# Kernel optimization log

Measured on AMD Instinct MI355X. Metric: run time of the kernel, lower is better.

Reference implementation:

```python
import jax, jax.numpy as jnp
import numpy as np

N_NODES = 100000
N_GRAPHS = 64
EPS = 1e-5


def _sage_conv(x, src, dst, Wl, bl, Wr):
    # mean-aggregate neighbor messages (src -> dst), then lin_l(agg) + lin_r(x)
    n = x.shape[0]
    deg = jax.ops.segment_sum(jnp.ones_like(dst, dtype=x.dtype), dst, num_segments=n)
    agg = jax.ops.segment_sum(x[src], dst, num_segments=n)  # [N, d]
    agg = agg / jnp.maximum(deg, 1.0)[:, None]
    return agg @ Wl + bl + x @ Wr


def _bn_relu(x, gamma, beta):
    mu = jnp.mean(x, axis=0)
    var = jnp.var(x, axis=0)
    return jax.nn.relu((x - mu) * jax.lax.rsqrt(var + EPS) * gamma + beta)


def setup_inputs() -> dict:
    key = jax.random.key(0)
    ks = jax.random.split(key, 16)
    E = 1600000
    x = jax.random.normal(ks[0], (N_NODES, 2), dtype=jnp.float32)
    edge_index = jax.random.randint(ks[1], (2, E), 0, N_NODES, dtype=jnp.int64)
    batch = jnp.sort(jax.random.randint(ks[2], (N_NODES,), 0, N_GRAPHS, dtype=jnp.int64))

    def lin(k, din, dout):
        s = 1.0 / np.sqrt(din)
        return jax.random.uniform(k, (din, dout), jnp.float32, -s, s)

    d = {"x": x, "edge_index": edge_index, "batch": batch}
    dims = [(2, 32), (32, 64), (64, 128)]
    for i, (din, dout) in enumerate(dims, 1):
        k1, k2 = jax.random.split(ks[2 + i])
        d[f"Wl{i}"] = lin(k1, din, dout)
        d[f"bl{i}"] = jnp.zeros((dout,), jnp.float32)
        d[f"Wr{i}"] = lin(k2, din, dout)
        d[f"g{i}"] = jnp.ones((dout,), jnp.float32)
        d[f"be{i}"] = jnp.zeros((dout,), jnp.float32)
    d["Wf1"] = lin(ks[10], 128, 64)
    d["bf1"] = jnp.zeros((64,), jnp.float32)
    d["Wf2"] = lin(ks[11], 64, 1)
    d["bf2"] = jnp.zeros((1,), jnp.float32)
    return d


def reference(x, edge_index, batch,
              Wl1, bl1, Wr1, g1, be1,
              Wl2, bl2, Wr2, g2, be2,
              Wl3, bl3, Wr3, g3, be3,
              Wf1, bf1, Wf2, bf2):
    src, dst = edge_index[0], edge_index[1]
    h = _bn_relu(_sage_conv(x, src, dst, Wl1, bl1, Wr1), g1, be1)
    h = _bn_relu(_sage_conv(h, src, dst, Wl2, bl2, Wr2), g2, be2)
    h = _bn_relu(_sage_conv(h, src, dst, Wl3, bl3, Wr3), g3, be3)
    # global mean pool over graphs
    cnt = jax.ops.segment_sum(jnp.ones_like(batch, dtype=h.dtype), batch, num_segments=N_GRAPHS)
    pooled = jax.ops.segment_sum(h, batch, num_segments=N_GRAPHS) / jnp.maximum(cnt, 1.0)[:, None]
    out = jax.nn.relu(pooled @ Wf1 + bf1)
    # dropout is identity in eval mode
    return out @ Wf2 + bf2
```

## Files before the change

### kernel.cpp

```cpp
#include <hip/hip_runtime.h>
#include <hip/hip_fp16.h>

#define N_NODES 100000
#define N_GRAPHS 64
#define BN_EPS 1e-5

#define NB 782
#define NC 49
#define PT1 4096
#define PT2 2048
#define BPC 16
#define CAP 3072

__device__ __forceinline__ float bfly64(float v) {
#pragma unroll
    for (int m = 1; m < 64; m <<= 1) v += __shfl_xor(v, m, 64);
    return v;
}

__device__ __forceinline__ unsigned pack_h2(float a, float b) {
    __half2 h = __floats2half2_rn(a, b);
    unsigned w;
    __builtin_memcpy(&w, &h, 4);
    return w;
}

__device__ __forceinline__ float2 unpack_h2(unsigned w) {
    __half2 h;
    __builtin_memcpy(&h, &w, 4);
    return __half22float2(h);
}

__global__ void hist_fine(const int* __restrict__ dst, int* __restrict__ bhist, int E) {
    __shared__ int h[NB];
    for (int i = threadIdx.x; i < NB; i += 256) h[i] = 0;
    __syncthreads();
    int stride = gridDim.x * 256;
    for (int e = blockIdx.x * 256 + threadIdx.x; e < E; e += stride) {
        int d = __builtin_nontemporal_load(dst + e);
        atomicAdd(&h[d >> 7], 1);
    }
    __syncthreads();
    for (int i = threadIdx.x; i < NB; i += 256)
        if (h[i]) atomicAdd(&bhist[i], h[i]);
}

__global__ void scan_buckets(const int* __restrict__ bhist, int* __restrict__ bo,
                             int* __restrict__ fcur, int* __restrict__ co,
                             int* __restrict__ ccur) {
    __shared__ int sh[1024];
    int t = threadIdx.x;
    sh[t] = (t < NB) ? bhist[t] : 0;
    __syncthreads();
    for (int st = 1; st < 1024; st <<= 1) {
        int v = (t >= st) ? sh[t - st] : 0;
        __syncthreads();
        sh[t] += v;
        __syncthreads();
    }
    int total = sh[NB - 1];
    if (t < NB) {
        int e = t ? sh[t - 1] : 0;
        bo[t] = e; fcur[t] = e;
    } else if (t < 784) {
        if (t == NB) bo[NB] = total;
        fcur[t] = total;
    }
    if (t < NC) {
        int i = t << 4;
        int e = i ? sh[i - 1] : 0;
        co[t] = e; ccur[t] = e;
    } else if (t == NC) {
        co[NC] = total;
    }
}

__global__ __launch_bounds__(256)
void part1(const int* __restrict__ dst, const int* __restrict__ src,
           int* __restrict__ ccur, int* __restrict__ cdst, int* __restrict__ csrc, int E) {
    __shared__ int ld[PT1], ls[PT1];
    __shared__ unsigned char lb[PT1];
    __shared__ int hist[NC], lbase[NC], gbase[NC];
    long long t0 = (long long)blockIdx.x * PT1;
    int n = (int)min((long long)PT1, (long long)E - t0);
    int tid = threadIdx.x;
    for (int i = tid; i < NC; i += 256) hist[i] = 0;
    __syncthreads();
    int d[PT1 / 256], s[PT1 / 256], c[PT1 / 256];
#pragma unroll
    for (int k = 0; k < PT1 / 256; ++k) {
        int li = k * 256 + tid;
        if (li < n) {
            d[k] = __builtin_nontemporal_load(dst + t0 + li);
            s[k] = __builtin_nontemporal_load(src + t0 + li);
            c[k] = d[k] >> 11;
            atomicAdd(&hist[c[k]], 1);
        }
    }
    __syncthreads();
    if (tid == 0) {
        int run = 0;
        for (int i = 0; i < NC; ++i) { lbase[i] = run; run += hist[i]; }
    }
    __syncthreads();
    if (tid < NC) gbase[tid] = atomicAdd(&ccur[tid], hist[tid]);
    __syncthreads();
    for (int i = tid; i < NC; i += 256) hist[i] = 0;
    __syncthreads();
#pragma unroll
    for (int k = 0; k < PT1 / 256; ++k) {
        int li = k * 256 + tid;
        if (li < n) {
            int pos = lbase[c[k]] + atomicAdd(&hist[c[k]], 1);
            ld[pos] = d[k]; ls[pos] = s[k]; lb[pos] = (unsigned char)c[k];
        }
    }
    __syncthreads();
    for (int i = tid; i < n; i += 256) {
        int bb = lb[i];
        int g = gbase[bb] + (i - lbase[bb]);
        cdst[g] = ld[i];
        csrc[g] = ls[i];
    }
}

__global__ __launch_bounds__(256)
void part2(const int* __restrict__ cdst, const int* __restrict__ csrc,
           const int* __restrict__ co, int* __restrict__ fcur,
           int* __restrict__ qdst, int* __restrict__ qsrc) {
    __shared__ int ld[PT2], ls[PT2];
    __shared__ unsigned char lb[PT2];
    __shared__ int hist[16], lbase[16], gbase[16];
    int c = blockIdx.x / BPC;
    int j = blockIdx.x % BPC;
    int beg = co[c], end = co[c + 1];
    int tid = threadIdx.x;
    for (int t0 = beg + j * PT2; t0 < end; t0 += BPC * PT2) {
        int n = min(PT2, end - t0);
        if (tid < 16) hist[tid] = 0;
        __syncthreads();
        int d[PT2 / 256], s[PT2 / 256], f[PT2 / 256];
#pragma unroll
        for (int k = 0; k < PT2 / 256; ++k) {
            int li = k * 256 + tid;
            if (li < n) {
                d[k] = cdst[t0 + li];
                s[k] = csrc[t0 + li];
                f[k] = (d[k] >> 7) & 15;
                atomicAdd(&hist[f[k]], 1);
            }
        }
        __syncthreads();
        if (tid == 0) {
            int run = 0;
            for (int i = 0; i < 16; ++i) { lbase[i] = run; run += hist[i]; }
        }
        __syncthreads();
        if (tid < 16) gbase[tid] = atomicAdd(&fcur[(c << 4) + tid], hist[tid]);
        __syncthreads();
        if (tid < 16) hist[tid] = 0;
        __syncthreads();
#pragma unroll
        for (int k = 0; k < PT2 / 256; ++k) {
            int li = k * 256 + tid;
            if (li < n) {
                int pos = lbase[f[k]] + atomicAdd(&hist[f[k]], 1);
                ld[pos] = d[k]; ls[pos] = s[k]; lb[pos] = (unsigned char)f[k];
            }
        }
        __syncthreads();
        for (int i = tid; i < n; i += 256) {
            int bb = lb[i];
            int g = gbase[bb] + (i - lbase[bb]);
            qdst[g] = ld[i];
            qsrc[g] = ls[i];
        }
        __syncthreads();
    }
}

__global__ __launch_bounds__(256)
void fill_final(const int* __restrict__ qdst, const int* __restrict__ qsrc,
                const int* __restrict__ bo, int* __restrict__ offs,
                int* __restrict__ nbr, int N, int E) {
    __shared__ int cnt[128], cbase[128], cur[128];
    __shared__ int lout[CAP];
    int b = blockIdx.x;
    int nlo = b << 7;
    int nn = min(128, N - nlo);
    int ebeg = bo[b], ne = bo[b + 1] - ebeg;
    int tid = threadIdx.x;
    if (tid < 128) { cnt[tid] = 0; cur[tid] = 0; }
    __syncthreads();
    for (int i = tid; i < ne; i += 256)
        atomicAdd(&cnt[qdst[ebeg + i] - nlo], 1);
    __syncthreads();
    if (tid < 128) cbase[tid] = cnt[tid];
    __syncthreads();
    for (int st = 1; st < 128; st <<= 1) {
        int v = 0;
        if (tid < 128 && tid >= st) v = cbase[tid - st];
        __syncthreads();
        if (tid < 128 && tid >= st) cbase[tid] += v;
        __syncthreads();
    }
    if (tid < nn)
        offs[nlo + tid] = ebeg + (tid ? cbase[tid - 1] : 0);
    if (b == NB - 1 && tid == 0) offs[N] = E;
    __syncthreads();
    for (int i = tid; i < ne; i += 256) {
        int d = qdst[ebeg + i];
        int s = qsrc[ebeg + i];
        int ln = d - nlo;
        int p = (ln ? cbase[ln - 1] : 0) + atomicAdd(&cur[ln], 1);
        lout[p] = s;
    }
    __syncthreads();
    for (int i = tid; i < ne; i += 256)
        nbr[ebeg + i] = lout[i];
}

__global__ __launch_bounds__(256)
void layer1_fused(const float2* __restrict__ x2,
                  const int* __restrict__ offs, const int* __restrict__ nbr,
                  const float* __restrict__ Wl, const float* __restrict__ bl,
                  const float* __restrict__ Wr,
                  __half* __restrict__ hout16,
                  double* __restrict__ sums, int N) {
    __shared__ float sAr[64];
    int tid = threadIdx.x;
    if (tid < 64) sAr[tid] = 0.f;
    __syncthreads();
    int n = blockIdx.x * 256 + tid;
    bool valid = (n < N);
    int beg = 0, end = 0;
    if (valid) { beg = offs[n]; end = offs[n + 1]; }
    double ax = 0.0, ay = 0.0;
    int j = beg;
    for (; j + 4 <= end; j += 4) {
        int s0 = nbr[j], s1 = nbr[j + 1], s2 = nbr[j + 2], s3 = nbr[j + 3];
        float2 v0 = x2[s0], v1 = x2[s1], v2 = x2[s2], v3 = x2[s3];
        ax += v0.x; ay += v0.y;
        ax += v1.x; ay += v1.y;
        ax += v2.x; ay += v2.y;
        ax += v3.x; ay += v3.y;
    }
    for (; j < end; ++j) {
        float2 v = x2[nbr[j]];
        ax += v.x; ay += v.y;
    }
    float invd = 1.0f / fmaxf((float)(end - beg), 1.0f);
    float a0 = (float)ax * invd, a1 = (float)ay * invd;
    float x0 = 0.f, x1 = 0.f;
    if (valid) {
        float2 xv = x2[n];
        x0 = xv.x; x1 = xv.y;
    }
    float acc[32];
#pragma unroll
    for (int jj = 0; jj < 32; ++jj)
        acc[jj] = bl[jj] + a0 * Wl[jj] + a1 * Wl[32 + jj] + x0 * Wr[jj] + x1 * Wr[32 + jj];
    if (valid) {
        unsigned w[16];
#pragma unroll
        for (int p = 0; p < 16; ++p) w[p] = pack_h2(acc[2*p], acc[2*p+1]);
        uint4* q = (uint4*)(hout16 + (size_t)n * 32);
        q[0] = make_uint4(w[0], w[1], w[2], w[3]);
        q[1] = make_uint4(w[4], w[5], w[6], w[7]);
        q[2] = make_uint4(w[8], w[9], w[10], w[11]);
        q[3] = make_uint4(w[12], w[13], w[14], w[15]);
    }
    int lane = tid & 63;
#pragma unroll
    for (int jj = 0; jj < 32; ++jj) {
        float v = valid ? acc[jj] : 0.f;
        float s = bfly64(v);
        float q = bfly64(v * v);
        if (lane == jj) atomicAdd(&sAr[jj], s);
        if (lane == 32 + jj) atomicAdd(&sAr[32 + jj], q);
    }
    __syncthreads();
    if (tid < 64) atomicAdd(&sums[tid], (double)sAr[tid]);
}

template<int F>
__global__ __launch_bounds__(256)
void agg_h16(const uint2* __restrict__ xh, const int* __restrict__ offs,
             const int* __restrict__ nbr,
             const double* __restrict__ sums,
             const float* __restrict__ gamma, const float* __restrict__ beta,
             uint2* __restrict__ aggh, int N) {
    constexpr int FV = F / 4;
    constexpr int NPB = 256 / FV;
    __shared__ float lsc[F], lsf[F];
    int tid = threadIdx.y * FV + threadIdx.x;
    if (tid < F) {
        double mu = sums[tid] / (double)N_NODES;
        double var = sums[F + tid] / (double)N_NODES - mu * mu;
        if (var < 0.0) var = 0.0;
        double sc = (double)gamma[tid] / sqrt(var + BN_EPS);
        lsc[tid] = (float)sc;
        lsf[tid] = (float)((double)beta[tid] - mu * sc);
    }
    __syncthreads();
    int n = blockIdx.x * NPB + threadIdx.y;
    if (n >= N) return;
    int f = threadIdx.x;
    float4 sc = ((const float4*)lsc)[f];
    float4 sf = ((const float4*)lsf)[f];
    int beg = offs[n], end = offs[n + 1];
    double ax = 0.0, ay = 0.0, az = 0.0, aw = 0.0;
    int j = beg;
    for (; j + 8 <= end; j += 8) {
        int s[8];
#pragma unroll
        for (int u = 0; u < 8; ++u) s[u] = __builtin_nontemporal_load(nbr + j + u);
        uint2 uv[8];
#pragma unroll
        for (int u = 0; u < 8; ++u) uv[u] = xh[(long long)s[u] * FV + f];
#pragma unroll
        for (int u = 0; u < 8; ++u) {
            float2 f0 = unpack_h2(uv[u].x);
            float2 f1 = unpack_h2(uv[u].y);
            ax += fmaxf(f0.x * sc.x + sf.x, 0.f);
            ay += fmaxf(f0.y * sc.y + sf.y, 0.f);
            az += fmaxf(f1.x * sc.z + sf.z, 0.f);
            aw += fmaxf(f1.y * sc.w + sf.w, 0.f);
        }
    }
    for (; j + 4 <= end; j += 4) {
        int s[4];
#pragma unroll
        for (int u = 0; u < 4; ++u) s[u] = __builtin_nontemporal_load(nbr + j + u);
        uint2 uv[4];
#pragma unroll
        for (int u = 0; u < 4; ++u) uv[u] = xh[(long long)s[u] * FV + f];
#pragma unroll
        for (int u = 0; u < 4; ++u) {
            float2 f0 = unpack_h2(uv[u].x);
            float2 f1 = unpack_h2(uv[u].y);
            ax += fmaxf(f0.x * sc.x + sf.x, 0.f);
            ay += fmaxf(f0.y * sc.y + sf.y, 0.f);
            az += fmaxf(f1.x * sc.z + sf.z, 0.f);
            aw += fmaxf(f1.y * sc.w + sf.w, 0.f);
        }
    }
    for (; j < end; ++j) {
        int s = __builtin_nontemporal_load(nbr + j);
        uint2 uv = xh[(long long)s * FV + f];
        float2 f0 = unpack_h2(uv.x);
        float2 f1 = unpack_h2(uv.y);
        ax += fmaxf(f0.x * sc.x + sf.x, 0.f);
        ay += fmaxf(f0.y * sc.y + sf.y, 0.f);
        az += fmaxf(f1.x * sc.z + sf.z, 0.f);
        aw += fmaxf(f1.y * sc.w + sf.w, 0.f);
    }
    uint2 out;
    out.x = pack_h2((float)ax, (float)ay);
    out.y = pack_h2((float)az, (float)aw);
    aggh[(long long)n * FV + f] = out;
}

template<int DIN, int DOUT, int TN>
__global__ __launch_bounds__(256)
void linear_t2(const __half* __restrict__ xin16, const __half* __restrict__ agg16,
               const int* __restrict__ offs,
               const float* __restrict__ Wl, const float* __restrict__ bl,
               const float* __restrict__ Wr,
               const double* __restrict__ sumsIn,
               const float* __restrict__ gIn, const float* __restrict__ beIn,
               __half* __restrict__ hout16, int N) {
    constexpr int JT = 32;
    constexpr int NG = DOUT / JT;
    static_assert(TN * NG == 256, "cfg");
    constexpr int STRIDE = DIN + 1;
    constexpr int DIV4 = DIN / 4;
    constexpr int NV4 = TN * DIN / 4;
    __shared__ float shT[TN * STRIDE];
    __shared__ float shD[TN];
    __shared__ float lscIn[DIN], lsfIn[DIN];

    int tid = threadIdx.x;
    if (tid < DIN) {
        double mu = sumsIn[tid] / (double)N_NODES;
        double var = sumsIn[DIN + tid] / (double)N_NODES - mu * mu;
        if (var < 0.0) var = 0.0;
        double sc = (double)gIn[tid] / sqrt(var + BN_EPS);
        lscIn[tid] = (float)sc;
        lsfIn[tid] = (float)((double)beIn[tid] - mu * sc);
    }

    int n0 = blockIdx.x * TN;
    const uint2* __restrict__ gA = (const uint2*)(agg16 + (size_t)n0 * DIN);
#pragma unroll
    for (int it = 0; it < NV4 / 256; ++it) {
        int i = it * 256 + tid;
        int row = i / DIV4, col = (i % DIV4) * 4;
        uint2 uv = gA[i];
        float2 f0 = unpack_h2(uv.x);
        float2 f1 = unpack_h2(uv.y);
        float* p = &shT[row * STRIDE + col];
        p[0] = f0.x; p[1] = f0.y; p[2] = f1.x; p[3] = f1.y;
    }
    for (int i = tid; i < TN; i += 256) {
        int nn = min(n0 + i, N - 1);
        shD[i] = 1.0f / fmaxf((float)(offs[nn + 1] - offs[nn]), 1.0f);
    }
    __syncthreads();

    int tn = tid % TN;
    int jg = __builtin_amdgcn_readfirstlane(tid / TN);
    float invd = shD[tn];
    float acc[JT];
#pragma unroll
    for (int j = 0; j < JT; ++j) acc[j] = bl[jg * JT + j];

#pragma unroll 4
    for (int k = 0; k < DIN; ++k) {
        float a = shT[tn * STRIDE + k] * invd;
        const float* __restrict__ wlp = Wl + (size_t)k * DOUT + jg * JT;
#pragma unroll
        for (int j = 0; j < JT; ++j) acc[j] += a * wlp[j];
    }
    __syncthreads();

    const uint2* __restrict__ gX = (const uint2*)(xin16 + (size_t)n0 * DIN);
#pragma unroll
    for (int it = 0; it < NV4 / 256; ++it) {
        int i = it * 256 + tid;
        int row = i / DIV4, col4 = i % DIV4;
        uint2 uv = gX[i];
        float2 f0 = unpack_h2(uv.x);
        float2 f1 = unpack_h2(uv.y);
        float4 sc = ((const float4*)lscIn)[col4];
        float4 sf = ((const float4*)lsfIn)[col4];
        float* q = &shT[row * STRIDE + col4 * 4];
        q[0] = fmaxf(f0.x * sc.x + sf.x, 0.f);
        q[1] = fmaxf(f0.y * sc.y + sf.y, 0.f);
        q[2] = fmaxf(f1.x * sc.z + sf.z, 0.f);
        q[3] = fmaxf(f1.y * sc.w + sf.w, 0.f);
    }
    __syncthreads();

#pragma unroll 4
    for (int k = 0; k < DIN; ++k) {
        float xv = shT[tn * STRIDE + k];
        const float* __restrict__ wrp = Wr + (size_t)k * DOUT + jg * JT;
#pragma unroll
        for (int j = 0; j < JT; ++j) acc[j] += xv * wrp[j];
    }

    if (n0 + tn < N) {
        unsigned w[16];
#pragma unroll
        for (int p = 0; p < 16; ++p) w[p] = pack_h2(acc[2*p], acc[2*p+1]);
        uint4* qh = (uint4*)(hout16 + (size_t)(n0 + tn) * DOUT + jg * JT);
        qh[0] = make_uint4(w[0], w[1], w[2], w[3]);
        qh[1] = make_uint4(w[4], w[5], w[6], w[7]);
        qh[2] = make_uint4(w[8], w[9], w[10], w[11]);
        qh[3] = make_uint4(w[12], w[13], w[14], w[15]);
    }
}

template<int F>
__global__ __launch_bounds__(256)
void stats_partial(const uint4* __restrict__ h, float* __restrict__ partial, int N) {
    constexpr int P4 = F / 8;
    constexpr int R = 256 / P4;
    constexpr int NV = P4 * 16;
    __shared__ float lds[4 * NV];
    int tid = threadIdx.x;
    int p = tid % P4;
    int r = tid / P4;
    float s[8], q[8];
#pragma unroll
    for (int j = 0; j < 8; ++j) { s[j] = 0.f; q[j] = 0.f; }
    for (int n = blockIdx.x * R + r; n < N; n += 1024 * R) {
        uint4 v = h[(size_t)n * P4 + p];
        float2 a = unpack_h2(v.x), b = unpack_h2(v.y), c = unpack_h2(v.z), d = unpack_h2(v.w);
        s[0] += a.x; q[0] += a.x * a.x;
        s[1] += a.y; q[1] += a.y * a.y;
        s[2] += b.x; q[2] += b.x * b.x;
        s[3] += b.y; q[3] += b.y * b.y;
        s[4] += c.x; q[4] += c.x * c.x;
        s[5] += c.y; q[5] += c.y * c.y;
        s[6] += d.x; q[6] += d.x * d.x;
        s[7] += d.y; q[7] += d.y * d.y;
    }
    for (int m = P4; m < 64; m <<= 1) {
#pragma unroll
        for (int j = 0; j < 8; ++j) {
            s[j] += __shfl_xor(s[j], m, 64);
            q[j] += __shfl_xor(q[j], m, 64);
        }
    }
    int wave = tid >> 6;
    int lane = tid & 63;
    if (lane < P4) {
#pragma unroll
        for (int j = 0; j < 8; ++j) {
            lds[wave * NV + lane * 16 + j] = s[j];
            lds[wave * NV + lane * 16 + 8 + j] = q[j];
        }
    }
    __syncthreads();
    for (int v = tid; v < NV; v += 256) {
        float t0 = lds[v] + lds[NV + v] + lds[2 * NV + v] + lds[3 * NV + v];
        int pp = v >> 4, k = v & 15;
        int feat = pp * 8 + (k & 7);
        int out = (k < 8) ? feat : (F + feat);
        partial[(size_t)blockIdx.x * (2 * F) + out] = t0;
    }
}

template<int F>
__global__ __launch_bounds__(256)
void stats_finalize(const float* __restrict__ partial, double* __restrict__ sums) {
    __shared__ double sh[256];
    int i = blockIdx.x;
    int t = threadIdx.x;
    double a = 0.0;
#pragma unroll
    for (int k = 0; k < 4; ++k)
        a += (double)partial[(size_t)(t + k * 256) * (2 * F) + i];
    sh[t] = a;
    __syncthreads();
    for (int st = 128; st > 0; st >>= 1) {
        if (t < st) sh[t] += sh[t + st];
        __syncthreads();
    }
    if (t == 0) sums[i] = sh[0];
}

__global__ void pool_partial(const __half* __restrict__ h, const int* __restrict__ batch,
                             const double* __restrict__ sums,
                             const float* __restrict__ gamma, const float* __restrict__ beta,
                             double* __restrict__ pooled_d, int N) {
    __shared__ float lsc[128], lsf[128];
    const int CH = 64;
    int f = threadIdx.x;
    {
        double mu = sums[f] / (double)N_NODES;
        double var = sums[128 + f] / (double)N_NODES - mu * mu;
        if (var < 0.0) var = 0.0;
        double sc = (double)gamma[f] / sqrt(var + BN_EPS);
        lsc[f] = (float)sc;
        lsf[f] = (float)((double)beta[f] - mu * sc);
    }
    __syncthreads();
    int n0 = blockIdx.x * CH;
    if (n0 >= N) return;
    int n1 = min(n0 + CH, N);
    float sc = lsc[f], sf = lsf[f];
    int g = batch[n0];
    float acc = 0.f;
    for (int n = n0; n < n1; ++n) {
        int bg = batch[n];
        if (bg != g) {
            atomicAdd(&pooled_d[g * 128 + f], (double)acc);
            acc = 0.f;
            g = bg;
        }
        float v = __half2float(h[(long long)n * 128 + f]);
        acc += fmaxf(v * sc + sf, 0.f);
    }
    atomicAdd(&pooled_d[g * 128 + f], (double)acc);
}

__global__ void mlp_fused(const double* __restrict__ pooled_d, const int* __restrict__ batch,
                          const float* __restrict__ Wf1, const float* __restrict__ bf1,
                          const float* __restrict__ Wf2, const float* __restrict__ bf2,
                          float* __restrict__ out, int N) {
    __shared__ float sp[128];
    int g = blockIdx.x;
    int t = threadIdx.x;
    int lo = 0, hi = N;
    while (lo < hi) { int m = (lo + hi) >> 1; if (batch[m] < g) lo = m + 1; else hi = m; }
    int start = lo;
    hi = N;
    while (lo < hi) { int m = (lo + hi) >> 1; if (batch[m] < g + 1) lo = m + 1; else hi = m; }
    int cnt = lo - start;
    sp[t] = (float)(pooled_d[g * 128 + t] / (double)max(cnt, 1));
    __syncthreads();
    if (t < 64) {
        float hacc = bf1[t];
#pragma unroll 8
        for (int k = 0; k < 128; ++k) hacc += sp[k] * Wf1[k * 64 + t];
        hacc = fmaxf(hacc, 0.f) * Wf2[t];
        for (int o = 32; o > 0; o >>= 1) hacc += __shfl_down(hacc, o);
        if (t == 0) out[g] = hacc + bf2[0];
    }
}

extern "C" void kernel_launch(void* const* d_in, const int* in_sizes, int n_in,
                              void* d_out, int out_size, void* d_ws, size_t ws_size,
                              hipStream_t stream) {
    const float* x     = (const float*)d_in[0];
    const int*   ei    = (const int*)d_in[1];
    const int*   batch = (const int*)d_in[2];
    const float *Wl1=(const float*)d_in[3],  *bl1=(const float*)d_in[4],  *Wr1=(const float*)d_in[5];
    const float *g1 =(const float*)d_in[6],  *be1=(const float*)d_in[7];
    const float *Wl2=(const float*)d_in[8],  *bl2=(const float*)d_in[9],  *Wr2=(const float*)d_in[10];
    const float *g2 =(const float*)d_in[11], *be2=(const float*)d_in[12];
    const float *Wl3=(const float*)d_in[13], *bl3=(const float*)d_in[14], *Wr3=(const float*)d_in[15];
    const float *g3 =(const float*)d_in[16], *be3=(const float*)d_in[17];
    const float *Wf1=(const float*)d_in[18], *bf1=(const float*)d_in[19];
    const float *Wf2=(const float*)d_in[20], *bf2=(const float*)d_in[21];

    const int N = N_NODES;
    const int E = in_sizes[1] / 2;
    const int* src = ei;
    const int* dst = ei + E;

    char* ws = (char*)d_ws;
    size_t off = 0;
    auto salloc = [&](size_t bytes) {
        void* p = ws + off;
        off += (bytes + 255) & ~(size_t)255;
        return p;
    };
    int*    bhist   = (int*)   salloc(NB * 4);
    double* sums    = (double*)salloc(768 * 8);
    double* pooledd = (double*)salloc((size_t)N_GRAPHS * 128 * 8);
    size_t zero_bytes = off;
    int*    offs    = (int*)   salloc((size_t)(N + 1) * 4);
    int*    bo      = (int*)   salloc((NB + 1) * 4);
    int*    fcur    = (int*)   salloc(784 * 4);
    int*    co      = (int*)   salloc((NC + 1) * 4);
    int*    ccur    = (int*)   salloc(NC * 4);
    int*    nbr     = (int*)   salloc((size_t)E * 4);
    float*  partial = (float*) salloc((size_t)1024 * 256 * 4);
    __half* h1h     = (__half*)salloc((size_t)(N + 256) * 32 * 2);
    __half* h2h     = (__half*)salloc((size_t)(N + 256) * 64 * 2);
    __half* h3h     = (__half*)salloc((size_t)(N + 256) * 128 * 2);
    __half* aggh    = (__half*)salloc((size_t)(N + 256) * 64 * 2);
    (void)ws_size;

    double* sums1 = sums, *sums2 = sums + 256, *sums3 = sums + 512;
    int* cdst = (int*)h3h;
    int* csrc = cdst + E;
    int* qdst = (int*)aggh;
    int* qsrc = qdst + E;

    hipMemsetAsync(bhist, 0, zero_bytes, stream);

    hist_fine<<<1024, 256, 0, stream>>>(dst, bhist, E);
    scan_buckets<<<1, 1024, 0, stream>>>(bhist, bo, fcur, co, ccur);
    part1<<<(E + PT1 - 1) / PT1, 256, 0, stream>>>(dst, src, ccur, cdst, csrc, E);
    part2<<<NC * BPC, 256, 0, stream>>>(cdst, csrc, co, fcur, qdst, qsrc);
    fill_final<<<NB, 256, 0, stream>>>(qdst, qsrc, bo, offs, nbr, N, E);

    const int NL = (N + 255) / 256;

    layer1_fused<<<NL, 256, 0, stream>>>((const float2*)x, offs, nbr,
                                          Wl1, bl1, Wr1, h1h, sums1, N);

    agg_h16<32><<<(N + 31) / 32, dim3(8, 32), 0, stream>>>(
        (const uint2*)h1h, offs, nbr, sums1, g1, be1, (uint2*)aggh, N);
    linear_t2<32, 64, 128><<<(N + 127) / 128, 256, 0, stream>>>(
        h1h, aggh, offs, Wl2, bl2, Wr2, sums1, g1, be1, h2h, N);
    stats_partial<64><<<1024, 256, 0, stream>>>((const uint4*)h2h, partial, N);
    stats_finalize<64><<<128, 256, 0, stream>>>(partial, sums2);

    agg_h16<64><<<(N + 15) / 16, dim3(16, 16), 0, stream>>>(
        (const uint2*)h2h, offs, nbr, sums2, g2, be2, (uint2*)aggh, N);
    linear_t2<64, 128, 64><<<(N + 63) / 64, 256, 0, stream>>>(
        h2h, aggh, offs, Wl3, bl3, Wr3, sums2, g2, be2, h3h, N);
    stats_partial<128><<<1024, 256, 0, stream>>>((const uint4*)h3h, partial, N);
    stats_finalize<128><<<256, 256, 0, stream>>>(partial, sums3);

    pool_partial<<<(N + 63) / 64, 128, 0, stream>>>(h3h, batch, sums3, g3, be3, pooledd, N);
    mlp_fused<<<N_GRAPHS, 128, 0, stream>>>(pooledd, batch, Wf1, bf1, Wf2, bf2, (float*)d_out, N);
}
```

Before: 377.1 us.

## Fuse neighbor mean aggregation into the linear layer kernels for layers 2 and 3

Removes the separate agg_h16 kernels and does the gather-sum of BN+ReLU'd neighbor features directly inside the linear kernel, writing normalized mean aggregates to shared memory before the matmul. This avoids writing and rereading the fp16 aggregate buffer and saves two launches. The cost is that the gather is now done by fewer, larger blocks (128/64 nodes per block, looped), so there may be less parallelism and latency hiding for the irregular gathers. The aggregate is also no longer rounded to fp16. A separate buffer is now allocated for the partition scratch that used to alias aggh.

```diff
diff --git a/kernel.cpp b/kernel.cpp
--- a/kernel.cpp
+++ b/kernel.cpp
@@ -283,101 +283,24 @@
     if (tid < 64) atomicAdd(&sums[tid], (double)sAr[tid]);
 }
 
-template<int F>
-__global__ __launch_bounds__(256)
-void agg_h16(const uint2* __restrict__ xh, const int* __restrict__ offs,
-             const int* __restrict__ nbr,
-             const double* __restrict__ sums,
-             const float* __restrict__ gamma, const float* __restrict__ beta,
-             uint2* __restrict__ aggh, int N) {
-    constexpr int FV = F / 4;
-    constexpr int NPB = 256 / FV;
-    __shared__ float lsc[F], lsf[F];
-    int tid = threadIdx.y * FV + threadIdx.x;
-    if (tid < F) {
-        double mu = sums[tid] / (double)N_NODES;
-        double var = sums[F + tid] / (double)N_NODES - mu * mu;
-        if (var < 0.0) var = 0.0;
-        double sc = (double)gamma[tid] / sqrt(var + BN_EPS);
-        lsc[tid] = (float)sc;
-        lsf[tid] = (float)((double)beta[tid] - mu * sc);
-    }
-    __syncthreads();
-    int n = blockIdx.x * NPB + threadIdx.y;
-    if (n >= N) return;
-    int f = threadIdx.x;
-    float4 sc = ((const float4*)lsc)[f];
-    float4 sf = ((const float4*)lsf)[f];
-    int beg = offs[n], end = offs[n + 1];
-    double ax = 0.0, ay = 0.0, az = 0.0, aw = 0.0;
-    int j = beg;
-    for (; j + 8 <= end; j += 8) {
-        int s[8];
-#pragma unroll
-        for (int u = 0; u < 8; ++u) s[u] = __builtin_nontemporal_load(nbr + j + u);
-        uint2 uv[8];
-#pragma unroll
-        for (int u = 0; u < 8; ++u) uv[u] = xh[(long long)s[u] * FV + f];
-#pragma unroll
-        for (int u = 0; u < 8; ++u) {
-            float2 f0 = unpack_h2(uv[u].x);
-            float2 f1 = unpack_h2(uv[u].y);
-            ax += fmaxf(f0.x * sc.x + sf.x, 0.f);
-            ay += fmaxf(f0.y * sc.y + sf.y, 0.f);
-            az += fmaxf(f1.x * sc.z + sf.z, 0.f);
-            aw += fmaxf(f1.y * sc.w + sf.w, 0.f);
-        }
-    }
-    for (; j + 4 <= end; j += 4) {
-        int s[4];
-#pragma unroll
-        for (int u = 0; u < 4; ++u) s[u] = __builtin_nontemporal_load(nbr + j + u);
-        uint2 uv[4];
-#pragma unroll
-        for (int u = 0; u < 4; ++u) uv[u] = xh[(long long)s[u] * FV + f];
-#pragma unroll
-        for (int u = 0; u < 4; ++u) {
-            float2 f0 = unpack_h2(uv[u].x);
-            float2 f1 = unpack_h2(uv[u].y);
-            ax += fmaxf(f0.x * sc.x + sf.x, 0.f);
-            ay += fmaxf(f0.y * sc.y + sf.y, 0.f);
-            az += fmaxf(f1.x * sc.z + sf.z, 0.f);
-            aw += fmaxf(f1.y * sc.w + sf.w, 0.f);
-        }
-    }
-    for (; j < end; ++j) {
-        int s = __builtin_nontemporal_load(nbr + j);
-        uint2 uv = xh[(long long)s * FV + f];
-        float2 f0 = unpack_h2(uv.x);
-        float2 f1 = unpack_h2(uv.y);
-        ax += fmaxf(f0.x * sc.x + sf.x, 0.f);
-        ay += fmaxf(f0.y * sc.y + sf.y, 0.f);
-        az += fmaxf(f1.x * sc.z + sf.z, 0.f);
-        aw += fmaxf(f1.y * sc.w + sf.w, 0.f);
-    }
-    uint2 out;
-    out.x = pack_h2((float)ax, (float)ay);
-    out.y = pack_h2((float)az, (float)aw);
-    aggh[(long long)n * FV + f] = out;
-}
-
 template<int DIN, int DOUT, int TN>
 __global__ __launch_bounds__(256)
-void linear_t2(const __half* __restrict__ xin16, const __half* __restrict__ agg16,
-               const int* __restrict__ offs,
-               const float* __restrict__ Wl, const float* __restrict__ bl,
-               const float* __restrict__ Wr,
-               const double* __restrict__ sumsIn,
-               const float* __restrict__ gIn, const float* __restrict__ beIn,
-               __half* __restrict__ hout16, int N) {
+void linear_f(const __half* __restrict__ xin16,
+              const int* __restrict__ offs, const int* __restrict__ nbr,
+              const float* __restrict__ Wl, const float* __restrict__ bl,
+              const float* __restrict__ Wr,
+              const double* __restrict__ sumsIn,
+              const float* __restrict__ gIn, const float* __restrict__ beIn,
+              __half* __restrict__ hout16, int N) {
     constexpr int JT = 32;
     constexpr int NG = DOUT / JT;
     static_assert(TN * NG == 256, "cfg");
     constexpr int STRIDE = DIN + 1;
     constexpr int DIV4 = DIN / 4;
     constexpr int NV4 = TN * DIN / 4;
+    constexpr int FV = DIN / 4;
+    constexpr int NPG = 256 / FV;
     __shared__ float shT[TN * STRIDE];
-    __shared__ float shD[TN];
     __shared__ float lscIn[DIN], lsfIn[DIN];
 
     int tid = threadIdx.x;
@@ -389,35 +312,85 @@
         lscIn[tid] = (float)sc;
         lsfIn[tid] = (float)((double)beIn[tid] - mu * sc);
     }
+    __syncthreads();
 
     int n0 = blockIdx.x * TN;
-    const uint2* __restrict__ gA = (const uint2*)(agg16 + (size_t)n0 * DIN);
-#pragma unroll
-    for (int it = 0; it < NV4 / 256; ++it) {
-        int i = it * 256 + tid;
-        int row = i / DIV4, col = (i % DIV4) * 4;
-        uint2 uv = gA[i];
-        float2 f0 = unpack_h2(uv.x);
-        float2 f1 = unpack_h2(uv.y);
-        float* p = &shT[row * STRIDE + col];
-        p[0] = f0.x; p[1] = f0.y; p[2] = f1.x; p[3] = f1.y;
-    }
-    for (int i = tid; i < TN; i += 256) {
-        int nn = min(n0 + i, N - 1);
-        shD[i] = 1.0f / fmaxf((float)(offs[nn + 1] - offs[nn]), 1.0f);
+    {
+        int fg = tid % FV;
+        float4 sc = ((const float4*)lscIn)[fg];
+        float4 sf = ((const float4*)lsfIn)[fg];
+        const uint2* __restrict__ xh = (const uint2*)xin16;
+#pragma unroll 1
+        for (int base = 0; base < TN; base += NPG) {
+            int ln = base + tid / FV;
+            int n = n0 + ln;
+            int beg = 0, end = 0;
+            if (n < N) { beg = offs[n]; end = offs[n + 1]; }
+            double ax = 0.0, ay = 0.0, az = 0.0, aw = 0.0;
+            int j = beg;
+            for (; j + 8 <= end; j += 8) {
+                int s[8];
+#pragma unroll
+                for (int u = 0; u < 8; ++u) s[u] = __builtin_nontemporal_load(nbr + j + u);
+                uint2 uv[8];
+#pragma unroll
+                for (int u = 0; u < 8; ++u) uv[u] = xh[(long long)s[u] * FV + fg];
+#pragma unroll
+                for (int u = 0; u < 8; ++u) {
+                    float2 f0 = unpack_h2(uv[u].x);
+                    float2 f1 = unpack_h2(uv[u].y);
+                    ax += fmaxf(f0.x * sc.x + sf.x, 0.f);
+                    ay += fmaxf(f0.y * sc.y + sf.y, 0.f);
+                    az += fmaxf(f1.x * sc.z + sf.z, 0.f);
+                    aw += fmaxf(f1.y * sc.w + sf.w, 0.f);
+                }
+            }
+            for (; j + 4 <= end; j += 4) {
+                int s[4];
+#pragma unroll
+                for (int u = 0; u < 4; ++u) s[u] = __builtin_nontemporal_load(nbr + j + u);
+                uint2 uv[4];
+#pragma unroll
+                for (int u = 0; u < 4; ++u) uv[u] = xh[(long long)s[u] * FV + fg];
+#pragma unroll
+                for (int u = 0; u < 4; ++u) {
+                    float2 f0 = unpack_h2(uv[u].x);
+                    float2 f1 = unpack_h2(uv[u].y);
+                    ax += fmaxf(f0.x * sc.x + sf.x, 0.f);
+                    ay += fmaxf(f0.y * sc.y + sf.y, 0.f);
+                    az += fmaxf(f1.x * sc.z + sf.z, 0.f);
+                    aw += fmaxf(f1.y * sc.w + sf.w, 0.f);
+                }
+            }
+            for (; j < end; ++j) {
+                int s = __builtin_nontemporal_load(nbr + j);
+                uint2 uv = xh[(long long)s * FV + fg];
+                float2 f0 = unpack_h2(uv.x);
+                float2 f1 = unpack_h2(uv.y);
+                ax += fmaxf(f0.x * sc.x + sf.x, 0.f);
+                ay += fmaxf(f0.y * sc.y + sf.y, 0.f);
+                az += fmaxf(f1.x * sc.z + sf.z, 0.f);
+                aw += fmaxf(f1.y * sc.w + sf.w, 0.f);
+            }
+            float invd = 1.0f / fmaxf((float)(end - beg), 1.0f);
+            float* p = &shT[ln * STRIDE + fg * 4];
+            p[0] = (float)ax * invd;
+            p[1] = (float)ay * invd;
+            p[2] = (float)az * invd;
+            p[3] = (float)aw * invd;
+        }
     }
     __syncthreads();
 
     int tn = tid % TN;
     int jg = __builtin_amdgcn_readfirstlane(tid / TN);
-    float invd = shD[tn];
     float acc[JT];
 #pragma unroll
     for (int j = 0; j < JT; ++j) acc[j] = bl[jg * JT + j];
 
 #pragma unroll 4
     for (int k = 0; k < DIN; ++k) {
-        float a = shT[tn * STRIDE + k] * invd;
+        float a = shT[tn * STRIDE + k];
         const float* __restrict__ wlp = Wl + (size_t)k * DOUT + jg * JT;
 #pragma unroll
         for (int j = 0; j < JT; ++j) acc[j] += a * wlp[j];
@@ -633,14 +606,14 @@
     __half* h1h     = (__half*)salloc((size_t)(N + 256) * 32 * 2);
     __half* h2h     = (__half*)salloc((size_t)(N + 256) * 64 * 2);
     __half* h3h     = (__half*)salloc((size_t)(N + 256) * 128 * 2);
-    __half* aggh    = (__half*)salloc((size_t)(N + 256) * 64 * 2);
+    int*    qbuf    = (int*)   salloc((size_t)2 * E * 4);
     (void)ws_size;
 
     double* sums1 = sums, *sums2 = sums + 256, *sums3 = sums + 512;
     int* cdst = (int*)h3h;
     int* csrc = cdst + E;
-    int* qdst = (int*)aggh;
-    int* qsrc = qdst + E;
+    int* qdst = qbuf;
+    int* qsrc = qbuf + E;
 
     hipMemsetAsync(bhist, 0, zero_bytes, stream);
 
@@ -655,17 +628,13 @@
     layer1_fused<<<NL, 256, 0, stream>>>((const float2*)x, offs, nbr,
                                           Wl1, bl1, Wr1, h1h, sums1, N);
 
-    agg_h16<32><<<(N + 31) / 32, dim3(8, 32), 0, stream>>>(
-        (const uint2*)h1h, offs, nbr, sums1, g1, be1, (uint2*)aggh, N);
-    linear_t2<32, 64, 128><<<(N + 127) / 128, 256, 0, stream>>>(
-        h1h, aggh, offs, Wl2, bl2, Wr2, sums1, g1, be1, h2h, N);
+    linear_f<32, 64, 128><<<(N + 127) / 128, 256, 0, stream>>>(
+        h1h, offs, nbr, Wl2, bl2, Wr2, sums1, g1, be1, h2h, N);
     stats_partial<64><<<1024, 256, 0, stream>>>((const uint4*)h2h, partial, N);
     stats_finalize<64><<<128, 256, 0, stream>>>(partial, sums2);
 
-    agg_h16<64><<<(N + 15) / 16, dim3(16, 16), 0, stream>>>(
-        (const uint2*)h2h, offs, nbr, sums2, g2, be2, (uint2*)aggh, N);
-    linear_t2<64, 128, 64><<<(N + 63) / 64, 256, 0, stream>>>(
-        h2h, aggh, offs, Wl3, bl3, Wr3, sums2, g2, be2, h3h, N);
+    linear_f<64, 128, 64><<<(N + 63) / 64, 256, 0, stream>>>(
+        h2h, offs, nbr, Wl3, bl3, Wr3, sums2, g2, be2, h3h, N);
     stats_partial<128><<<1024, 256, 0, stream>>>((const uint4*)h3h, partial, N);
     stats_finalize<128><<<256, 256, 0, stream>>>(partial, sums3);
 
```

After: 382.9 us. About the same (+1.6%).
